# Kernel optimization log

Hardware: AMD Instinct MI355X
Metric: run time of the kernel (lower is better)

Reference implementation:

```python
import jax, jax.numpy as jnp
import numpy as np

FP8_MAX = 448.0  # e4m3fn max


def _fake_quant_fp8(x, scale):
    # quantize: scale, clamp, round-trip through float8_e4m3fn; dequantize by 1/scale
    xq = jnp.clip(x * scale, -FP8_MAX, FP8_MAX).astype(jnp.float8_e4m3fn)
    return xq.astype(jnp.float32) * (1.0 / scale)


def _compute_scale(x):
    amax = jnp.max(jnp.abs(x))
    return FP8_MAX / jnp.maximum(amax, 1e-12)


def setup_inputs() -> dict:
    key = jax.random.key(0)
    kx, kw = jax.random.split(key)
    x = jax.random.normal(kx, (8, 2048, 4096), dtype=jnp.float32)
    weight = jax.random.normal(kw, (4096, 4096), dtype=jnp.float32) * 0.02
    return {"x": x, "weight": weight}


def reference(x, weight):
    B, S, K = x.shape
    N = weight.shape[1]
    # weight path: per-tensor scale, fp8 round-trip (transpose in original is value-preserving)
    w_dq = _fake_quant_fp8(weight, _compute_scale(weight))  # [K, N]
    # activation path
    x2d = x.reshape(-1, K)  # [M, K]
    x_dq = _fake_quant_fp8(x2d, _compute_scale(x2d))
    out = x_dq @ w_dq  # fp32 GEMM, [M, N]
    return out.reshape(B, S, N)
```

## Files before the change

### kernel.cpp

```cpp
#include <hip/hip_runtime.h>
#include <stdint.h>

#define FP8_MAX 448.0f

typedef float f32x4 __attribute__((ext_vector_type(4)));
typedef int i32x8 __attribute__((ext_vector_type(8)));
typedef int i32x4 __attribute__((ext_vector_type(4)));

__device__ __forceinline__ unsigned int pack4_fp8(float4 v, float s) {
  float a = fminf(fmaxf(v.x * s, -FP8_MAX), FP8_MAX);
  float b = fminf(fmaxf(v.y * s, -FP8_MAX), FP8_MAX);
  float c = fminf(fmaxf(v.z * s, -FP8_MAX), FP8_MAX);
  float d = fminf(fmaxf(v.w * s, -FP8_MAX), FP8_MAX);
  unsigned int r = (unsigned int)__builtin_amdgcn_cvt_pk_fp8_f32(a, b, 0, false);
  r = (unsigned int)__builtin_amdgcn_cvt_pk_fp8_f32(c, d, (int)r, true);
  return r;
}

__device__ __forceinline__ void load16_to_lds(const void* g, void* l) {
  auto gp = (const __attribute__((address_space(1))) void*)(uintptr_t)g;
  auto lp = (__attribute__((address_space(3))) void*)(unsigned int)(uintptr_t)l;
  __builtin_amdgcn_global_load_lds(gp, lp, 16, 0, 0);
}

__device__ __forceinline__ float amax4(float4 v) {
  return fmaxf(fmaxf(fabsf(v.x), fabsf(v.y)), fmaxf(fabsf(v.z), fabsf(v.w)));
}

__global__ void amax2_kernel(const float* __restrict__ x, int n4x,
                             const float* __restrict__ w, int n4w,
                             unsigned int* __restrict__ hdr) {
  const float4* p4;
  int n4, base, nblk;
  unsigned int* slot;
  if (blockIdx.x < 2048) {
    p4 = (const float4*)x; n4 = n4x; base = blockIdx.x; nblk = 2048; slot = hdr;
  } else {
    p4 = (const float4*)w; n4 = n4w; base = blockIdx.x - 2048; nblk = 512; slot = hdr + 1;
  }
  int stride = nblk * blockDim.x;
  int i = base * blockDim.x + threadIdx.x;
  float m = 0.0f;
  for (; i + 3 * stride < n4; i += 4 * stride) {
    float4 v0 = p4[i];
    float4 v1 = p4[i + stride];
    float4 v2 = p4[i + 2 * stride];
    float4 v3 = p4[i + 3 * stride];
    m = fmaxf(m, fmaxf(fmaxf(amax4(v0), amax4(v1)), fmaxf(amax4(v2), amax4(v3))));
  }
  for (; i < n4; i += stride) m = fmaxf(m, amax4(p4[i]));
#pragma unroll
  for (int off = 32; off > 0; off >>= 1)
    m = fmaxf(m, __shfl_down(m, off, 64));
  __shared__ float wmax[4];
  int lane = threadIdx.x & 63;
  int wv = threadIdx.x >> 6;
  if (lane == 0) wmax[wv] = m;
  __syncthreads();
  if (threadIdx.x == 0) {
    m = fmaxf(fmaxf(wmax[0], wmax[1]), fmaxf(wmax[2], wmax[3]));
    atomicMax(slot, __float_as_uint(m));
  }
}

__global__ void quant_fused_kernel(const float* __restrict__ x, unsigned int* __restrict__ xq,
                                   int n16x,
                                   const float* __restrict__ w, unsigned char* __restrict__ wqT,
                                   int K, int N, const unsigned int* __restrict__ hdr) {
  __shared__ unsigned int tileT[64][17];
  if (blockIdx.x < 2048) {
    float s = FP8_MAX / fmaxf(__uint_as_float(hdr[0]), 1e-12f);
    const float4* x4 = (const float4*)x;
    uint4* o4 = (uint4*)xq;
    int stride = 2048 * blockDim.x;
    for (int i = blockIdx.x * blockDim.x + threadIdx.x; i < n16x; i += stride) {
      float4 a = x4[4 * i + 0];
      float4 b = x4[4 * i + 1];
      float4 c = x4[4 * i + 2];
      float4 d = x4[4 * i + 3];
      o4[i] = make_uint4(pack4_fp8(a, s), pack4_fp8(b, s), pack4_fp8(c, s), pack4_fp8(d, s));
    }
  } else {
    float s = FP8_MAX / fmaxf(__uint_as_float(hdr[1]), 1e-12f);
    int bx = blockIdx.x - 2048;
    int tn0 = (bx & 63) << 6;
    int tk0 = (bx >> 6) << 6;
    int t = threadIdx.x;

    int rn = (t & 15) << 2;
    int rk = (t >> 4) << 2;
    unsigned int wrow[4];
#pragma unroll
    for (int j = 0; j < 4; ++j) {
      float4 v = *(const float4*)(w + (size_t)(tk0 + rk + j) * N + tn0 + rn);
      wrow[j] = pack4_fp8(v, s);
    }
#pragma unroll
    for (int i = 0; i < 4; ++i) {
      unsigned int colw = ((wrow[0] >> (8 * i)) & 0xffu)
                        | (((wrow[1] >> (8 * i)) & 0xffu) << 8)
                        | (((wrow[2] >> (8 * i)) & 0xffu) << 16)
                        | (((wrow[3] >> (8 * i)) & 0xffu) << 24);
      tileT[rn + i][rk >> 2] = colw;
    }
    __syncthreads();

    int n = t >> 2;
    int kc = (t & 3) << 2;
    uint4 v = make_uint4(tileT[n][kc], tileT[n][kc + 1], tileT[n][kc + 2], tileT[n][kc + 3]);
    *(uint4*)(wqT + (size_t)(tn0 + n) * K + tk0 + (kc << 2)) = v;
  }
}

__device__ __forceinline__ i32x8 read_frag(const unsigned char* p, int off0) {
  i32x4 lo = *(const i32x4*)(p + off0);
  i32x4 hi = *(const i32x4*)(p + (off0 ^ 16));
  return __builtin_shufflevector(lo, hi, 0, 1, 2, 3, 4, 5, 6, 7);
}

#define MFMA1(a, b, c) \
  __builtin_amdgcn_mfma_scale_f32_16x16x128_f8f6f4(a, b, c, 0, 0, 0, 0x7f7f7f7f, 0, 0x7f7f7f7f)

#define MFMA_Q(M0_, N0_)                                              \
  do {                                                                \
    __builtin_amdgcn_s_setprio(1);                                    \
    acc[M0_ + 0][N0_ + 0] = MFMA1(af[0], bf[N0_ + 0], acc[M0_ + 0][N0_ + 0]); \
    acc[M0_ + 0][N0_ + 1] = MFMA1(af[0], bf[N0_ + 1], acc[M0_ + 0][N0_ + 1]); \
    acc[M0_ + 1][N0_ + 0] = MFMA1(af[1], bf[N0_ + 0], acc[M0_ + 1][N0_ + 0]); \
    acc[M0_ + 1][N0_ + 1] = MFMA1(af[1], bf[N0_ + 1], acc[M0_ + 1][N0_ + 1]); \
    acc[M0_ + 2][N0_ + 0] = MFMA1(af[2], bf[N0_ + 0], acc[M0_ + 2][N0_ + 0]); \
    acc[M0_ + 2][N0_ + 1] = MFMA1(af[2], bf[N0_ + 1], acc[M0_ + 2][N0_ + 1]); \
    acc[M0_ + 3][N0_ + 0] = MFMA1(af[3], bf[N0_ + 0], acc[M0_ + 3][N0_ + 0]); \
    acc[M0_ + 3][N0_ + 1] = MFMA1(af[3], bf[N0_ + 1], acc[M0_ + 3][N0_ + 1]); \
    __builtin_amdgcn_s_setprio(0);                                    \
  } while (0)

#define BAR() __builtin_amdgcn_s_barrier()
#define LGKM0()                                           \
  do {                                                    \
    asm volatile("s_waitcnt lgkmcnt(0)" ::: "memory");    \
    __builtin_amdgcn_sched_barrier(0);                    \
  } while (0)
#define VMCNT(N_)                                               \
  do {                                                          \
    asm volatile("s_waitcnt vmcnt(" #N_ ")" ::: "memory");      \
    __builtin_amdgcn_sched_barrier(0);                          \
  } while (0)

__global__ __launch_bounds__(512, 2) void gemm_fp8_kernel(
    const unsigned char* __restrict__ Aq,
    const unsigned char* __restrict__ Bq,
    const unsigned int* __restrict__ hdr,
    float* __restrict__ out, int M, int N, int K) {
  __shared__ __align__(16) unsigned char smem[131072];

  const int t = threadIdx.x;
  const int wave = t >> 6;
  const int lane = t & 63;
  const int row16 = lane & 15;
  const int quad = lane >> 4;
  const int wr = wave >> 2;
  const int wc = wave & 3;
  const int m0 = blockIdx.y << 8;
  const int n0 = blockIdx.x << 8;

  const int sRow = (wave << 3) + (lane >> 3);
  const int sCol = (((lane & 7) ^ (lane >> 3)) << 4);
  const unsigned char* agBase = Aq + (size_t)(m0 + sRow) * K + sCol;
  const unsigned char* bgBase = Bq + (size_t)(n0 + sRow) * K + sCol;
  const int ldsStageOff = (wave << 10) + (lane << 4);

  auto stageA = [&](int u, int h) {
    const int buf = (u & 1) << 15;
#pragma unroll
    for (int r = 0; r < 2; ++r)
      load16_to_lds(agBase + (size_t)((h << 7) + (r << 6)) * K + ((size_t)u << 7),
                    smem + buf + (h << 14) + (r << 13) + ldsStageOff);
  };
  auto stageB = [&](int u, int h) {
    const int buf = (u & 1) << 15;
#pragma unroll
    for (int r = 0; r < 2; ++r)
      load16_to_lds(bgBase + (size_t)((h << 7) + (r << 6)) * K + ((size_t)u << 7),
                    smem + 65536 + buf + (h << 14) + (r << 13) + ldsStageOff);
  };

  const int off0 = (((quad << 1) ^ (row16 & 7)) << 4);
  const int aRow = (wr << 7) + row16;
  const int bRow = (wc << 6) + row16;

  f32x4 acc[8][4] = {};

  const int NT = K >> 7;

  stageA(0, 0); stageA(0, 1); stageB(0, 0); stageB(0, 1);
  stageA(1, 0); stageB(1, 0);
  VMCNT(4);
  BAR();

  auto tile_body = [&](int tt, bool stg1, bool stg2, int waitN) {
    const int buf = (tt & 1) << 15;
    const unsigned char* Ab = smem + buf;
    const unsigned char* Bb = smem + 65536 + buf;
    i32x8 af[4], bf[4];
    af[0] = read_frag(Ab + ((aRow + 0) << 7), off0);
    af[1] = read_frag(Ab + ((aRow + 16) << 7), off0);
    af[2] = read_frag(Ab + ((aRow + 32) << 7), off0);
    af[3] = read_frag(Ab + ((aRow + 48) << 7), off0);
    bf[0] = read_frag(Bb + ((bRow + 0) << 7), off0);
    bf[1] = read_frag(Bb + ((bRow + 16) << 7), off0);
    if (stg1) stageA(tt + 1, 1);
    BAR();
    LGKM0();
    MFMA_Q(0, 0);
    BAR();
    bf[2] = read_frag(Bb + ((bRow + 32) << 7), off0);
    bf[3] = read_frag(Bb + ((bRow + 48) << 7), off0);
    if (stg1) stageB(tt + 1, 1);
    BAR();
    LGKM0();
    MFMA_Q(0, 2);
    BAR();
    af[0] = read_frag(Ab + ((aRow + 64) << 7), off0);
    af[1] = read_frag(Ab + ((aRow + 80) << 7), off0);
    af[2] = read_frag(Ab + ((aRow + 96) << 7), off0);
    af[3] = read_frag(Ab + ((aRow + 112) << 7), off0);
    if (stg2) stageB(tt + 2, 0);
    BAR();
    LGKM0();
    MFMA_Q(4, 0);
    BAR();
    if (stg2) stageA(tt + 2, 0);
    if (waitN == 4) {
      VMCNT(4);
    } else if (waitN == 0) {
      VMCNT(0);
    }
    BAR();
    MFMA_Q(4, 2);
    BAR();
  };

  for (int tt = 0; tt < NT - 2; ++tt) tile_body(tt, true, true, 4);
  tile_body(NT - 2, true, false, 0);
  tile_body(NT - 1, false, false, -1);

  const float ax = fmaxf(__uint_as_float(hdr[0]), 1e-12f);
  const float aw = fmaxf(__uint_as_float(hdr[1]), 1e-12f);
  const float sc = (ax / FP8_MAX) * (aw / FP8_MAX);
#pragma unroll
  for (int mi = 0; mi < 8; ++mi) {
#pragma unroll
    for (int ni = 0; ni < 4; ++ni) {
      const int gc = n0 + (wc << 6) + ni * 16 + row16;
#pragma unroll
      for (int r = 0; r < 4; ++r) {
        const int gr = m0 + (wr << 7) + mi * 16 + quad * 4 + r;
        out[(size_t)gr * N + gc] = acc[mi][ni][r] * sc;
      }
    }
  }
}

extern "C" void kernel_launch(void* const* d_in, const int* in_sizes, int n_in,
                              void* d_out, int out_size, void* d_ws, size_t ws_size,
                              hipStream_t stream) {
  const float* x = (const float*)d_in[0];
  const float* w = (const float*)d_in[1];
  float* out = (float*)d_out;

  const int K = 4096;
  const int N = 4096;
  const int M = in_sizes[0] / K;

  unsigned int* hdr = (unsigned int*)d_ws;
  unsigned char* xq = (unsigned char*)d_ws + 16;
  unsigned char* wqT = xq + (size_t)M * K;

  hipMemsetAsync(d_ws, 0, 16, stream);

  amax2_kernel<<<2560, 256, 0, stream>>>(x, (int)((size_t)M * K / 4), w,
                                         (int)((size_t)K * N / 4), hdr);

  quant_fused_kernel<<<2048 + 4096, 256, 0, stream>>>(
      x, (unsigned int*)xq, (int)((size_t)M * K / 16), w, wqT, K, N, hdr);

  gemm_fp8_kernel<<<dim3(N / 256, M / 256), 512, 0, stream>>>(xq, wqT, hdr, out, M, N, K);
}
```

Baseline: 797.0 us.

## Simplify GEMM pipeline to one-barrier double buffer; replace amax atomics with partials

```diff
diff --git a/kernel.cpp b/kernel.cpp
--- a/kernel.cpp
+++ b/kernel.cpp
@@ -27,16 +27,27 @@
   return fmaxf(fmaxf(fabsf(v.x), fabsf(v.y)), fmaxf(fabsf(v.z), fabsf(v.w)));
 }
 
+__device__ __forceinline__ float block_reduce_max256(float m, float* wred) {
+#pragma unroll
+  for (int off = 32; off > 0; off >>= 1)
+    m = fmaxf(m, __shfl_down(m, off, 64));
+  int lane = threadIdx.x & 63;
+  int wv = threadIdx.x >> 6;
+  if (lane == 0) wred[wv] = m;
+  __syncthreads();
+  return fmaxf(fmaxf(wred[0], wred[1]), fmaxf(wred[2], wred[3]));
+}
+
 __global__ void amax2_kernel(const float* __restrict__ x, int n4x,
                              const float* __restrict__ w, int n4w,
-                             unsigned int* __restrict__ hdr) {
+                             float* __restrict__ partials) {
+  __shared__ float wred[4];
   const float4* p4;
   int n4, base, nblk;
-  unsigned int* slot;
   if (blockIdx.x < 2048) {
-    p4 = (const float4*)x; n4 = n4x; base = blockIdx.x; nblk = 2048; slot = hdr;
+    p4 = (const float4*)x; n4 = n4x; base = blockIdx.x; nblk = 2048;
   } else {
-    p4 = (const float4*)w; n4 = n4w; base = blockIdx.x - 2048; nblk = 512; slot = hdr + 1;
+    p4 = (const float4*)w; n4 = n4w; base = blockIdx.x - 2048; nblk = 512;
   }
   int stride = nblk * blockDim.x;
   int i = base * blockDim.x + threadIdx.x;
@@ -49,27 +60,35 @@
     m = fmaxf(m, fmaxf(fmaxf(amax4(v0), amax4(v1)), fmaxf(amax4(v2), amax4(v3))));
   }
   for (; i < n4; i += stride) m = fmaxf(m, amax4(p4[i]));
-#pragma unroll
-  for (int off = 32; off > 0; off >>= 1)
-    m = fmaxf(m, __shfl_down(m, off, 64));
-  __shared__ float wmax[4];
-  int lane = threadIdx.x & 63;
-  int wv = threadIdx.x >> 6;
-  if (lane == 0) wmax[wv] = m;
-  __syncthreads();
-  if (threadIdx.x == 0) {
-    m = fmaxf(fmaxf(wmax[0], wmax[1]), fmaxf(wmax[2], wmax[3]));
-    atomicMax(slot, __float_as_uint(m));
-  }
+  m = block_reduce_max256(m, wred);
+  if (threadIdx.x == 0) partials[blockIdx.x] = m;
 }
 
 __global__ void quant_fused_kernel(const float* __restrict__ x, unsigned int* __restrict__ xq,
                                    int n16x,
                                    const float* __restrict__ w, unsigned char* __restrict__ wqT,
-                                   int K, int N, const unsigned int* __restrict__ hdr) {
+                                   int K, int N,
+                                   const float* __restrict__ partials,
+                                   float* __restrict__ hdrf) {
+  __shared__ float wred[4];
   __shared__ unsigned int tileT[64][17];
-  if (blockIdx.x < 2048) {
-    float s = FP8_MAX / fmaxf(__uint_as_float(hdr[0]), 1e-12f);
+  const bool isX = blockIdx.x < 2048;
+  const float* pp = isX ? partials : partials + 2048;
+  const int np = isX ? 2048 : 512;
+  float pm = 0.0f;
+  for (int i = threadIdx.x; i < np; i += 256) pm = fmaxf(pm, pp[i]);
+  float am = block_reduce_max256(pm, wred);
+  float s = FP8_MAX / fmaxf(am, 1e-12f);
+
+  if (blockIdx.x == 0) {
+    __syncthreads();
+    float pw = 0.0f;
+    for (int i = threadIdx.x; i < 512; i += 256) pw = fmaxf(pw, partials[2048 + i]);
+    float aw = block_reduce_max256(pw, wred);
+    if (threadIdx.x == 0) { hdrf[0] = am; hdrf[1] = aw; }
+  }
+
+  if (isX) {
     const float4* x4 = (const float4*)x;
     uint4* o4 = (uint4*)xq;
     int stride = 2048 * blockDim.x;
@@ -81,7 +100,6 @@
       o4[i] = make_uint4(pack4_fp8(a, s), pack4_fp8(b, s), pack4_fp8(c, s), pack4_fp8(d, s));
     }
   } else {
-    float s = FP8_MAX / fmaxf(__uint_as_float(hdr[1]), 1e-12f);
     int bx = blockIdx.x - 2048;
     int tn0 = (bx & 63) << 6;
     int tk0 = (bx >> 6) << 6;
@@ -121,36 +139,27 @@
 #define MFMA1(a, b, c) \
   __builtin_amdgcn_mfma_scale_f32_16x16x128_f8f6f4(a, b, c, 0, 0, 0, 0x7f7f7f7f, 0, 0x7f7f7f7f)
 
-#define MFMA_Q(M0_, N0_)                                              \
-  do {                                                                \
-    __builtin_amdgcn_s_setprio(1);                                    \
-    acc[M0_ + 0][N0_ + 0] = MFMA1(af[0], bf[N0_ + 0], acc[M0_ + 0][N0_ + 0]); \
-    acc[M0_ + 0][N0_ + 1] = MFMA1(af[0], bf[N0_ + 1], acc[M0_ + 0][N0_ + 1]); \
-    acc[M0_ + 1][N0_ + 0] = MFMA1(af[1], bf[N0_ + 0], acc[M0_ + 1][N0_ + 0]); \
-    acc[M0_ + 1][N0_ + 1] = MFMA1(af[1], bf[N0_ + 1], acc[M0_ + 1][N0_ + 1]); \
-    acc[M0_ + 2][N0_ + 0] = MFMA1(af[2], bf[N0_ + 0], acc[M0_ + 2][N0_ + 0]); \
-    acc[M0_ + 2][N0_ + 1] = MFMA1(af[2], bf[N0_ + 1], acc[M0_ + 2][N0_ + 1]); \
-    acc[M0_ + 3][N0_ + 0] = MFMA1(af[3], bf[N0_ + 0], acc[M0_ + 3][N0_ + 0]); \
-    acc[M0_ + 3][N0_ + 1] = MFMA1(af[3], bf[N0_ + 1], acc[M0_ + 3][N0_ + 1]); \
-    __builtin_amdgcn_s_setprio(0);                                    \
+#define MFMA_Q(AF_, B0_, B1_, M0_, N0_)                                   \
+  do {                                                                    \
+    acc[M0_ + 0][N0_ + 0] = MFMA1(AF_[0], B0_, acc[M0_ + 0][N0_ + 0]);    \
+    acc[M0_ + 0][N0_ + 1] = MFMA1(AF_[0], B1_, acc[M0_ + 0][N0_ + 1]);    \
+    acc[M0_ + 1][N0_ + 0] = MFMA1(AF_[1], B0_, acc[M0_ + 1][N0_ + 0]);    \
+    acc[M0_ + 1][N0_ + 1] = MFMA1(AF_[1], B1_, acc[M0_ + 1][N0_ + 1]);    \
+    acc[M0_ + 2][N0_ + 0] = MFMA1(AF_[2], B0_, acc[M0_ + 2][N0_ + 0]);    \
+    acc[M0_ + 2][N0_ + 1] = MFMA1(AF_[2], B1_, acc[M0_ + 2][N0_ + 1]);    \
+    acc[M0_ + 3][N0_ + 0] = MFMA1(AF_[3], B0_, acc[M0_ + 3][N0_ + 0]);    \
+    acc[M0_ + 3][N0_ + 1] = MFMA1(AF_[3], B1_, acc[M0_ + 3][N0_ + 1]);    \
   } while (0)
 
 #define BAR() __builtin_amdgcn_s_barrier()
-#define LGKM0()                                           \
-  do {                                                    \
-    asm volatile("s_waitcnt lgkmcnt(0)" ::: "memory");    \
-    __builtin_amdgcn_sched_barrier(0);                    \
-  } while (0)
-#define VMCNT(N_)                                               \
-  do {                                                          \
-    asm volatile("s_waitcnt vmcnt(" #N_ ")" ::: "memory");      \
-    __builtin_amdgcn_sched_barrier(0);                          \
-  } while (0)
+#define SCHED0() __builtin_amdgcn_sched_barrier(0)
+#define LGKM0() asm volatile("s_waitcnt lgkmcnt(0)" ::: "memory")
+#define VMCNT0() asm volatile("s_waitcnt vmcnt(0)" ::: "memory")
 
 __global__ __launch_bounds__(512, 2) void gemm_fp8_kernel(
     const unsigned char* __restrict__ Aq,
     const unsigned char* __restrict__ Bq,
-    const unsigned int* __restrict__ hdr,
+    const float* __restrict__ hdrf,
     float* __restrict__ out, int M, int N, int K) {
   __shared__ __align__(16) unsigned char smem[131072];
 
@@ -170,19 +179,17 @@
   const unsigned char* bgBase = Bq + (size_t)(n0 + sRow) * K + sCol;
   const int ldsStageOff = (wave << 10) + (lane << 4);
 
-  auto stageA = [&](int u, int h) {
+  auto stageT = [&](int u) {
     const int buf = (u & 1) << 15;
 #pragma unroll
-    for (int r = 0; r < 2; ++r)
-      load16_to_lds(agBase + (size_t)((h << 7) + (r << 6)) * K + ((size_t)u << 7),
-                    smem + buf + (h << 14) + (r << 13) + ldsStageOff);
-  };
-  auto stageB = [&](int u, int h) {
-    const int buf = (u & 1) << 15;
-#pragma unroll
-    for (int r = 0; r < 2; ++r)
-      load16_to_lds(bgBase + (size_t)((h << 7) + (r << 6)) * K + ((size_t)u << 7),
-                    smem + 65536 + buf + (h << 14) + (r << 13) + ldsStageOff);
+    for (int h = 0; h < 2; ++h)
+#pragma unroll
+      for (int r = 0; r < 2; ++r) {
+        load16_to_lds(agBase + (size_t)((h << 7) + (r << 6)) * K + ((size_t)u << 7),
+                      smem + buf + (h << 14) + (r << 13) + ldsStageOff);
+        load16_to_lds(bgBase + (size_t)((h << 7) + (r << 6)) * K + ((size_t)u << 7),
+                      smem + 65536 + buf + (h << 14) + (r << 13) + ldsStageOff);
+      }
   };
 
   const int off0 = (((quad << 1) ^ (row16 & 7)) << 4);
@@ -193,60 +200,44 @@
 
   const int NT = K >> 7;
 
-  stageA(0, 0); stageA(0, 1); stageB(0, 0); stageB(0, 1);
-  stageA(1, 0); stageB(1, 0);
-  VMCNT(4);
+  stageT(0);
+  VMCNT0();
   BAR();
 
-  auto tile_body = [&](int tt, bool stg1, bool stg2, int waitN) {
+  for (int tt = 0; tt < NT; ++tt) {
     const int buf = (tt & 1) << 15;
     const unsigned char* Ab = smem + buf;
     const unsigned char* Bb = smem + 65536 + buf;
-    i32x8 af[4], bf[4];
-    af[0] = read_frag(Ab + ((aRow + 0) << 7), off0);
-    af[1] = read_frag(Ab + ((aRow + 16) << 7), off0);
-    af[2] = read_frag(Ab + ((aRow + 32) << 7), off0);
-    af[3] = read_frag(Ab + ((aRow + 48) << 7), off0);
+    const bool more = (tt + 1 < NT);
+
+    if (more) stageT(tt + 1);
+    SCHED0();
+
+    i32x8 afA[4], afB[4], bf[4];
+    afA[0] = read_frag(Ab + ((aRow + 0) << 7), off0);
+    afA[1] = read_frag(Ab + ((aRow + 16) << 7), off0);
+    afA[2] = read_frag(Ab + ((aRow + 32) << 7), off0);
+    afA[3] = read_frag(Ab + ((aRow + 48) << 7), off0);
     bf[0] = read_frag(Bb + ((bRow + 0) << 7), off0);
     bf[1] = read_frag(Bb + ((bRow + 16) << 7), off0);
-    if (stg1) stageA(tt + 1, 1);
-    BAR();
-    LGKM0();
-    MFMA_Q(0, 0);
-    BAR();
+    MFMA_Q(afA, bf[0], bf[1], 0, 0);
     bf[2] = read_frag(Bb + ((bRow + 32) << 7), off0);
     bf[3] = read_frag(Bb + ((bRow + 48) << 7), off0);
-    if (stg1) stageB(tt + 1, 1);
+    MFMA_Q(afA, bf[2], bf[3], 0, 2);
+    afB[0] = read_frag(Ab + ((aRow + 64) << 7), off0);
+    afB[1] = read_frag(Ab + ((aRow + 80) << 7), off0);
+    afB[2] = read_frag(Ab + ((aRow + 96) << 7), off0);
+    afB[3] = read_frag(Ab + ((aRow + 112) << 7), off0);
+    MFMA_Q(afB, bf[0], bf[1], 4, 0);
+    MFMA_Q(afB, bf[2], bf[3], 4, 2);
+
+    LGKM0();
+    if (more) VMCNT0();
     BAR();
-    LGKM0();
-    MFMA_Q(0, 2);
-    BAR();
-    af[0] = read_frag(Ab + ((aRow + 64) << 7), off0);
-    af[1] = read_frag(Ab + ((aRow + 80) << 7), off0);
-    af[2] = read_frag(Ab + ((aRow + 96) << 7), off0);
-    af[3] = read_frag(Ab + ((aRow + 112) << 7), off0);
-    if (stg2) stageB(tt + 2, 0);
-    BAR();
-    LGKM0();
-    MFMA_Q(4, 0);
-    BAR();
-    if (stg2) stageA(tt + 2, 0);
-    if (waitN == 4) {
-      VMCNT(4);
-    } else if (waitN == 0) {
-      VMCNT(0);
-    }
-    BAR();
-    MFMA_Q(4, 2);
-    BAR();
-  };
-
-  for (int tt = 0; tt < NT - 2; ++tt) tile_body(tt, true, true, 4);
-  tile_body(NT - 2, true, false, 0);
-  tile_body(NT - 1, false, false, -1);
-
-  const float ax = fmaxf(__uint_as_float(hdr[0]), 1e-12f);
-  const float aw = fmaxf(__uint_as_float(hdr[1]), 1e-12f);
+  }
+
+  const float ax = fmaxf(hdrf[0], 1e-12f);
+  const float aw = fmaxf(hdrf[1], 1e-12f);
   const float sc = (ax / FP8_MAX) * (aw / FP8_MAX);
 #pragma unroll
   for (int mi = 0; mi < 8; ++mi) {
@@ -273,17 +264,16 @@
   const int N = 4096;
   const int M = in_sizes[0] / K;
 
-  unsigned int* hdr = (unsigned int*)d_ws;
-  unsigned char* xq = (unsigned char*)d_ws + 16;
+  float* partials = (float*)d_ws;
+  float* hdrf = (float*)((char*)d_ws + 12288);
+  unsigned char* xq = (unsigned char*)d_ws + 16384;
   unsigned char* wqT = xq + (size_t)M * K;
 
-  hipMemsetAsync(d_ws, 0, 16, stream);
-
   amax2_kernel<<<2560, 256, 0, stream>>>(x, (int)((size_t)M * K / 4), w,
-                                         (int)((size_t)K * N / 4), hdr);
+                                         (int)((size_t)K * N / 4), partials);
 
   quant_fused_kernel<<<2048 + 4096, 256, 0, stream>>>(
-      x, (unsigned int*)xq, (int)((size_t)M * K / 16), w, wqT, K, N, hdr);
-
-  gemm_fp8_kernel<<<dim3(N / 256, M / 256), 512, 0, stream>>>(xq, wqT, hdr, out, M, N, K);
-}
+      x, (unsigned int*)xq, (int)((size_t)M * K / 16), w, wqT, K, N, partials, hdrf);
+
+  gemm_fp8_kernel<<<dim3(N / 256, M / 256), 512, 0, stream>>>(xq, wqT, hdrf, out, M, N, K);
+}
```

Measured after the change: 801.5 us. Within noise of the previous version (+0.6%).
